# Kernel optimization log

Hardware: AMD Instinct MI355X
Metric: run time of the kernel (lower is better)

## Reference

```python
import jax, jax.numpy as jnp
import numpy as np

N_SRC = 50000
N_DST = 50000
N_EDGES = 600000
IN_FEAT = 128
OUT_FEAT = 128


def setup_inputs() -> dict:
    key = jax.random.key(0)
    k1, k2, k3, k4, k5, k6 = jax.random.split(key, 6)
    h_s = jax.random.normal(k1, (N_SRC, IN_FEAT), dtype=jnp.float32)
    h_d = jax.random.normal(k2, (N_DST, IN_FEAT), dtype=jnp.float32)
    src = jax.random.randint(k3, (N_EDGES,), 0, N_SRC, dtype=jnp.int32)
    dst = jax.random.randint(k4, (N_EDGES,), 0, N_DST, dtype=jnp.int32)
    # nn.Linear(in_feat*2, out_feat): W [out, 2*in], b [out]
    W = jax.random.normal(k5, (OUT_FEAT, 2 * IN_FEAT), dtype=jnp.float32) * 0.05
    b = jax.random.normal(k6, (OUT_FEAT,), dtype=jnp.float32) * 0.05
    return {"h_s": h_s, "h_d": h_d, "src": src, "dst": dst, "W": W, "b": b}


def reference(h_s, h_d, src, dst, W, b):
    # copy_u + mean: gather source features along edges, segment-mean by dst
    msgs = h_s[src]  # [E, in_feat]
    neigh_sum = jax.ops.segment_sum(msgs, dst, num_segments=N_DST)  # [n_dst, in_feat]
    deg = jax.ops.segment_sum(jnp.ones((src.shape[0],), dtype=h_s.dtype), dst,
                              num_segments=N_DST)
    h_neigh = neigh_sum / jnp.maximum(deg, 1.0)[:, None]  # zero-degree -> 0
    # concat + linear (dropout is identity in eval mode)
    feat = jnp.concatenate([h_d, h_neigh], axis=1)  # [n_dst, 2*in_feat]
    out = feat @ W.T + b  # [n_dst, out_feat]
    return out
```

## Files before the change

### kernel.cpp

```cpp
#include <hip/hip_runtime.h>
#include <hip/hip_bf16.h>

#define N_SRC 50000
#define N_DST 50000
#define N_EDGES 600000
#define IN_FEAT 128
#define OUT_FEAT 128
#define CAP 32
#define DEG_STRIDE 16

typedef __attribute__((ext_vector_type(8))) short short8;
typedef __attribute__((ext_vector_type(4))) float float4v;
typedef __attribute__((ext_vector_type(4))) float f32x4;
typedef __attribute__((ext_vector_type(4))) unsigned short ushort4v;

#define FILL_BLOCKS 2344
#define HS4 (N_SRC * IN_FEAT / 4)
#define CVT_BLOCKS (HS4 / 256)
#define W_BLOCKS 16
#define K1_GRID 15024

__global__ __launch_bounds__(256) void fill_cvt_kernel(
    const float* __restrict__ h_s, const float* __restrict__ h_d,
    const float* __restrict__ W,
    const int* __restrict__ src, const int* __restrict__ dst,
    int* __restrict__ deg, ushort* __restrict__ permu,
    ushort* __restrict__ hsb, ushort* __restrict__ hdb,
    ushort* __restrict__ wfrag)
{
    int bid = blockIdx.x;
    int tid = threadIdx.x;

    if (bid % 6 == 5) {
        int fb = bid / 6;
        if (fb >= FILL_BLOCKS) return;
        int e = fb * 256 + tid;
        if (e < N_EDGES) {
            int s = __builtin_nontemporal_load(src + e);
            int d = __builtin_nontemporal_load(dst + e);
            int p = atomicAdd(&deg[(size_t)d * DEG_STRIDE], 1);
            if (p < CAP) permu[(size_t)d * CAP + p] = (ushort)s;
        }
        return;
    }

    int cid = bid - bid / 6;

    if (cid < 2 * CVT_BLOCKS) {
        bool first = (cid < CVT_BLOCKS);
        const float* in = first ? h_s : h_d;
        ushort* outp    = first ? hsb : hdb;
        int idx = (first ? cid : cid - CVT_BLOCKS) * 256 + tid;
        f32x4 v = __builtin_nontemporal_load((const f32x4*)in + idx);
        __hip_bfloat16 o[4];
        o[0] = __float2bfloat16(v.x);
        o[1] = __float2bfloat16(v.y);
        o[2] = __float2bfloat16(v.z);
        o[3] = __float2bfloat16(v.w);
        __builtin_nontemporal_store(*(ushort4v*)o, (ushort4v*)(outp + (size_t)idx * 4));
        return;
    }
    int wb = cid - 2 * CVT_BLOCKS;
    if (wb >= W_BLOCKS) return;

    int c = wb * 256 + tid;
    int f  = c >> 6;
    int l  = c & 63;
    int ks = f >> 3;
    int nt = f & 7;
    int row = nt * 16 + (l & 15);
    int col = ks * 32 + (l >> 4) * 8;
    const float* wp = W + (size_t)row * 256 + col;
    f32x4 w0 = __builtin_nontemporal_load((const f32x4*)wp);
    f32x4 w1 = __builtin_nontemporal_load((const f32x4*)wp + 1);
    __hip_bfloat16 o[8];
    o[0] = __float2bfloat16(w0.x); o[1] = __float2bfloat16(w0.y);
    o[2] = __float2bfloat16(w0.z); o[3] = __float2bfloat16(w0.w);
    o[4] = __float2bfloat16(w1.x); o[5] = __float2bfloat16(w1.y);
    o[6] = __float2bfloat16(w1.z); o[7] = __float2bfloat16(w1.w);
    __builtin_nontemporal_store(*(short8*)o, (short8*)(wfrag + (size_t)c * 8));
}

__global__ __launch_bounds__(256) void gather_gemm_kernel(
    const ushort* __restrict__ hsb, const int* __restrict__ deg,
    const ushort* __restrict__ permu, const ushort* __restrict__ hdb,
    const ushort* __restrict__ wfrag, const float* __restrict__ b,
    float* __restrict__ out)
{
    __shared__ ushort sM[16 * 128];

    int tid  = threadIdx.x;
    int wave = tid >> 6;
    int lane = tid & 63;
    int lm   = lane & 15;
    int lq   = lane >> 4;
    int row0 = blockIdx.x * 16;

    for (int r = 0; r < 4; ++r) {
        int lr  = wave * 4 + r;
        int row = row0 + lr;
        int dg  = deg[(size_t)row * DEG_STRIDE];
        int dgr = (dg < CAP) ? dg : CAP;
        const ushort* prow = permu + (size_t)row * CAP;
        const ushort2* hp  = (const ushort2*)hsb;

        ushort4 p0 = *(const ushort4*)(prow);
        ushort4 p1 = *(const ushort4*)(prow + 4);
        ushort4 p2 = *(const ushort4*)(prow + 8);
        ushort4 p3 = *(const ushort4*)(prow + 12);
        int t[16] = {p0.x, p0.y, p0.z, p0.w, p1.x, p1.y, p1.z, p1.w,
                     p2.x, p2.y, p2.z, p2.w, p3.x, p3.y, p3.z, p3.w};

        float ax = 0.f, ay = 0.f;
        ushort2 u[16];
#pragma unroll
        for (int q = 0; q < 16; ++q) {
            int s = (q < dgr) ? t[q] : 0;
            u[q] = hp[(size_t)s * 64 + lane];
        }
#pragma unroll
        for (int q = 0; q < 16; ++q) {
            float m = (q < dgr) ? 1.f : 0.f;
            ax += m * __uint_as_float((unsigned)u[q].x << 16);
            ay += m * __uint_as_float((unsigned)u[q].y << 16);
        }
        for (int j = 16; j < dgr; j += 8) {
            ushort4 pa = *(const ushort4*)(prow + j);
            ushort4 pb = *(const ushort4*)(prow + j + 4);
            int tt[8] = {pa.x, pa.y, pa.z, pa.w, pb.x, pb.y, pb.z, pb.w};
            ushort2 v[8];
#pragma unroll
            for (int q = 0; q < 8; ++q) {
                int s = (j + q < dgr) ? tt[q] : 0;
                v[q] = hp[(size_t)s * 64 + lane];
            }
#pragma unroll
            for (int q = 0; q < 8; ++q) {
                float m = (j + q < dgr) ? 1.f : 0.f;
                ax += m * __uint_as_float((unsigned)v[q].x << 16);
                ay += m * __uint_as_float((unsigned)v[q].y << 16);
            }
        }

        float inv = (dg > 0) ? (1.0f / (float)dg) : 0.0f;
        __hip_bfloat16 ox = __float2bfloat16(ax * inv);
        __hip_bfloat16 oy = __float2bfloat16(ay * inv);
        unsigned pk = (unsigned)*(ushort*)&ox | ((unsigned)*(ushort*)&oy << 16);
        unsigned byte = ((unsigned)(lr * 256 + lane * 4)) ^ (((unsigned)lr & 7u) << 4);
        *(unsigned*)((char*)sM + byte) = pk;
    }
    __syncthreads();

    const ushort* ah = hdb + (size_t)(row0 + lm) * IN_FEAT + lq * 8;

    float4v acc[2];
    acc[0] = (float4v){0.f, 0.f, 0.f, 0.f};
    acc[1] = (float4v){0.f, 0.f, 0.f, 0.f};

#pragma unroll
    for (int ks = 0; ks < 8; ++ks) {
        short8 af;
        if (ks < 4) {
            af = __builtin_nontemporal_load((const short8*)(ah + ks * 32));
        } else {
            unsigned byte = ((unsigned)(lm * 256 + (((ks - 4) * 32 + lq * 8) * 2)))
                            ^ (((unsigned)lm & 7u) << 4);
            af = *(const short8*)((char*)sM + byte);
        }
#pragma unroll
        for (int j = 0; j < 2; ++j) {
            int nt = wave * 2 + j;
            short8 bf = *(const short8*)(wfrag + ((size_t)(ks * 8 + nt) * 64 + lane) * 8);
            acc[j] = __builtin_amdgcn_mfma_f32_16x16x32_bf16(af, bf, acc[j], 0, 0, 0);
        }
    }

#pragma unroll
    for (int j = 0; j < 2; ++j) {
        int nt  = wave * 2 + j;
        int col = nt * 16 + lm;
        float bias = b[col];
#pragma unroll
        for (int r = 0; r < 4; ++r) {
            int o = row0 + lq * 4 + r;
            __builtin_nontemporal_store(acc[j][r] + bias,
                                        out + (size_t)o * OUT_FEAT + col);
        }
    }
}

extern "C" void kernel_launch(void* const* d_in, const int* in_sizes, int n_in,
                              void* d_out, int out_size, void* d_ws, size_t ws_size,
                              hipStream_t stream) {
    const float* h_s = (const float*)d_in[0];
    const float* h_d = (const float*)d_in[1];
    const int*   src = (const int*)d_in[2];
    const int*   dst = (const int*)d_in[3];
    const float* W   = (const float*)d_in[4];
    const float* b   = (const float*)d_in[5];
    float* out = (float*)d_out;

    char* ws = (char*)d_ws;
    int*    deg    = (int*)ws;
    ushort* permu  = (ushort*)(ws + 3200000);
    ushort* hsb    = (ushort*)(ws + 6400000);
    ushort* hdb    = (ushort*)(ws + 19200000);
    ushort* wfrag  = (ushort*)(ws + 32000000);

    hipMemsetAsync(deg, 0, (size_t)N_DST * DEG_STRIDE * sizeof(int), stream);

    fill_cvt_kernel<<<K1_GRID, 256, 0, stream>>>(
        h_s, h_d, W, src, dst, deg, permu, hsb, hdb, wfrag);
    gather_gemm_kernel<<<N_DST / 16, 256, 0, stream>>>(
        hsb, deg, permu, hdb, wfrag, b, out);
}
```

Before: 171.6 us.

## Fuse fill/convert and gather-GEMM into one persistent kernel with grid barrier

Result: slower. 357.7 us (+108.5%).

```diff
diff --git a/kernel.cpp b/kernel.cpp
--- a/kernel.cpp
+++ b/kernel.cpp
@@ -9,183 +9,192 @@
 #define CAP 32
 #define DEG_STRIDE 16
 
+#define NBLK 1024
+#define NTHR 256
+#define NTHREADS (NBLK * NTHR)
+#define NTILES (N_DST / 16)
+#define HS4 (N_SRC * IN_FEAT / 4)
+
 typedef __attribute__((ext_vector_type(8))) short short8;
 typedef __attribute__((ext_vector_type(4))) float float4v;
 typedef __attribute__((ext_vector_type(4))) float f32x4;
 typedef __attribute__((ext_vector_type(4))) unsigned short ushort4v;
 
-#define FILL_BLOCKS 2344
-#define HS4 (N_SRC * IN_FEAT / 4)
-#define CVT_BLOCKS (HS4 / 256)
-#define W_BLOCKS 16
-#define K1_GRID 15024
-
-__global__ __launch_bounds__(256) void fill_cvt_kernel(
+__global__ __launch_bounds__(256, 4) void mega_kernel(
     const float* __restrict__ h_s, const float* __restrict__ h_d,
     const float* __restrict__ W,
     const int* __restrict__ src, const int* __restrict__ dst,
+    const float* __restrict__ b,
     int* __restrict__ deg, ushort* __restrict__ permu,
-    ushort* __restrict__ hsb, ushort* __restrict__ hdb,
-    ushort* __restrict__ wfrag)
+    ushort* __restrict__ hsb, ushort* __restrict__ wfrag,
+    int* __restrict__ bar, int* __restrict__ wcnt,
+    float* __restrict__ out)
 {
-    int bid = blockIdx.x;
+    __shared__ ushort sM[16 * 128];
+    __shared__ int sTile;
+
     int tid = threadIdx.x;
-
-    if (bid % 6 == 5) {
-        int fb = bid / 6;
-        if (fb >= FILL_BLOCKS) return;
-        int e = fb * 256 + tid;
-        if (e < N_EDGES) {
-            int s = __builtin_nontemporal_load(src + e);
-            int d = __builtin_nontemporal_load(dst + e);
-            int p = atomicAdd(&deg[(size_t)d * DEG_STRIDE], 1);
-            if (p < CAP) permu[(size_t)d * CAP + p] = (ushort)s;
-        }
-        return;
-    }
-
-    int cid = bid - bid / 6;
-
-    if (cid < 2 * CVT_BLOCKS) {
-        bool first = (cid < CVT_BLOCKS);
-        const float* in = first ? h_s : h_d;
-        ushort* outp    = first ? hsb : hdb;
-        int idx = (first ? cid : cid - CVT_BLOCKS) * 256 + tid;
-        f32x4 v = __builtin_nontemporal_load((const f32x4*)in + idx);
+    int gid = blockIdx.x * NTHR + tid;
+
+    for (int e = gid; e < N_EDGES; e += NTHREADS) {
+        int s = __builtin_nontemporal_load(src + e);
+        int d = __builtin_nontemporal_load(dst + e);
+        int p = atomicAdd(&deg[(size_t)d * DEG_STRIDE], 1);
+        if (p < CAP) permu[(size_t)d * CAP + p] = (ushort)s;
+    }
+
+    if (gid < 4096) {
+        int c  = gid;
+        int f  = c >> 6;
+        int l  = c & 63;
+        int ks = f >> 3;
+        int nt = f & 7;
+        int row = nt * 16 + (l & 15);
+        int col = ks * 32 + (l >> 4) * 8;
+        const float* wp = W + (size_t)row * 256 + col;
+        f32x4 w0 = __builtin_nontemporal_load((const f32x4*)wp);
+        f32x4 w1 = __builtin_nontemporal_load((const f32x4*)wp + 1);
+        __hip_bfloat16 o[8];
+        o[0] = __float2bfloat16(w0.x); o[1] = __float2bfloat16(w0.y);
+        o[2] = __float2bfloat16(w0.z); o[3] = __float2bfloat16(w0.w);
+        o[4] = __float2bfloat16(w1.x); o[5] = __float2bfloat16(w1.y);
+        o[6] = __float2bfloat16(w1.z); o[7] = __float2bfloat16(w1.w);
+        __builtin_nontemporal_store(*(short8*)o, (short8*)(wfrag + (size_t)c * 8));
+    }
+
+    for (int idx = gid; idx < HS4; idx += NTHREADS) {
+        f32x4 v = __builtin_nontemporal_load((const f32x4*)h_s + idx);
         __hip_bfloat16 o[4];
         o[0] = __float2bfloat16(v.x);
         o[1] = __float2bfloat16(v.y);
         o[2] = __float2bfloat16(v.z);
         o[3] = __float2bfloat16(v.w);
-        __builtin_nontemporal_store(*(ushort4v*)o, (ushort4v*)(outp + (size_t)idx * 4));
-        return;
-    }
-    int wb = cid - 2 * CVT_BLOCKS;
-    if (wb >= W_BLOCKS) return;
-
-    int c = wb * 256 + tid;
-    int f  = c >> 6;
-    int l  = c & 63;
-    int ks = f >> 3;
-    int nt = f & 7;
-    int row = nt * 16 + (l & 15);
-    int col = ks * 32 + (l >> 4) * 8;
-    const float* wp = W + (size_t)row * 256 + col;
-    f32x4 w0 = __builtin_nontemporal_load((const f32x4*)wp);
-    f32x4 w1 = __builtin_nontemporal_load((const f32x4*)wp + 1);
-    __hip_bfloat16 o[8];
-    o[0] = __float2bfloat16(w0.x); o[1] = __float2bfloat16(w0.y);
-    o[2] = __float2bfloat16(w0.z); o[3] = __float2bfloat16(w0.w);
-    o[4] = __float2bfloat16(w1.x); o[5] = __float2bfloat16(w1.y);
-    o[6] = __float2bfloat16(w1.z); o[7] = __float2bfloat16(w1.w);
-    __builtin_nontemporal_store(*(short8*)o, (short8*)(wfrag + (size_t)c * 8));
-}
-
-__global__ __launch_bounds__(256) void gather_gemm_kernel(
-    const ushort* __restrict__ hsb, const int* __restrict__ deg,
-    const ushort* __restrict__ permu, const ushort* __restrict__ hdb,
-    const ushort* __restrict__ wfrag, const float* __restrict__ b,
-    float* __restrict__ out)
-{
-    __shared__ ushort sM[16 * 128];
-
-    int tid  = threadIdx.x;
+        __builtin_nontemporal_store(*(ushort4v*)o, (ushort4v*)(hsb + (size_t)idx * 4));
+    }
+
+    __syncthreads();
+    if (tid == 0) {
+        __threadfence();
+        atomicAdd(bar, 1);
+        while (__hip_atomic_load(bar, __ATOMIC_RELAXED,
+                                 __HIP_MEMORY_SCOPE_AGENT) < NBLK)
+            __builtin_amdgcn_s_sleep(32);
+    }
+    __syncthreads();
+    __threadfence();
+
     int wave = tid >> 6;
     int lane = tid & 63;
     int lm   = lane & 15;
     int lq   = lane >> 4;
-    int row0 = blockIdx.x * 16;
-
-    for (int r = 0; r < 4; ++r) {
-        int lr  = wave * 4 + r;
-        int row = row0 + lr;
-        int dg  = deg[(size_t)row * DEG_STRIDE];
-        int dgr = (dg < CAP) ? dg : CAP;
-        const ushort* prow = permu + (size_t)row * CAP;
-        const ushort2* hp  = (const ushort2*)hsb;
-
-        ushort4 p0 = *(const ushort4*)(prow);
-        ushort4 p1 = *(const ushort4*)(prow + 4);
-        ushort4 p2 = *(const ushort4*)(prow + 8);
-        ushort4 p3 = *(const ushort4*)(prow + 12);
-        int t[16] = {p0.x, p0.y, p0.z, p0.w, p1.x, p1.y, p1.z, p1.w,
-                     p2.x, p2.y, p2.z, p2.w, p3.x, p3.y, p3.z, p3.w};
-
-        float ax = 0.f, ay = 0.f;
-        ushort2 u[16];
-#pragma unroll
-        for (int q = 0; q < 16; ++q) {
-            int s = (q < dgr) ? t[q] : 0;
-            u[q] = hp[(size_t)s * 64 + lane];
+
+    while (true) {
+        __syncthreads();
+        if (tid == 0) sTile = atomicAdd(wcnt, 1);
+        __syncthreads();
+        int t = sTile;
+        if (t >= NTILES) break;
+        int row0 = t * 16;
+
+        for (int r = 0; r < 4; ++r) {
+            int lr  = wave * 4 + r;
+            int row = row0 + lr;
+            int dg  = deg[(size_t)row * DEG_STRIDE];
+            int dgr = (dg < CAP) ? dg : CAP;
+            const ushort* prow = permu + (size_t)row * CAP;
+            const ushort2* hp  = (const ushort2*)hsb;
+
+            ushort4 p0 = *(const ushort4*)(prow);
+            ushort4 p1 = *(const ushort4*)(prow + 4);
+            ushort4 p2 = *(const ushort4*)(prow + 8);
+            ushort4 p3 = *(const ushort4*)(prow + 12);
+            int tt[16] = {p0.x, p0.y, p0.z, p0.w, p1.x, p1.y, p1.z, p1.w,
+                          p2.x, p2.y, p2.z, p2.w, p3.x, p3.y, p3.z, p3.w};
+
+            float ax = 0.f, ay = 0.f;
+            ushort2 u[16];
+#pragma unroll
+            for (int q = 0; q < 16; ++q) {
+                int s = (q < dgr) ? tt[q] : 0;
+                u[q] = hp[(size_t)s * 64 + lane];
+            }
+#pragma unroll
+            for (int q = 0; q < 16; ++q) {
+                float m = (q < dgr) ? 1.f : 0.f;
+                ax += m * __uint_as_float((unsigned)u[q].x << 16);
+                ay += m * __uint_as_float((unsigned)u[q].y << 16);
+            }
+            for (int j = 16; j < dgr; j += 8) {
+                ushort4 pa = *(const ushort4*)(prow + j);
+                ushort4 pb = *(const ushort4*)(prow + j + 4);
+                int t8[8] = {pa.x, pa.y, pa.z, pa.w, pb.x, pb.y, pb.z, pb.w};
+                ushort2 v[8];
+#pragma unroll
+                for (int q = 0; q < 8; ++q) {
+                    int s = (j + q < dgr) ? t8[q] : 0;
+                    v[q] = hp[(size_t)s * 64 + lane];
+                }
+#pragma unroll
+                for (int q = 0; q < 8; ++q) {
+                    float m = (j + q < dgr) ? 1.f : 0.f;
+                    ax += m * __uint_as_float((unsigned)v[q].x << 16);
+                    ay += m * __uint_as_float((unsigned)v[q].y << 16);
+                }
+            }
+
+            float inv = (dg > 0) ? (1.0f / (float)dg) : 0.0f;
+            __hip_bfloat16 ox = __float2bfloat16(ax * inv);
+            __hip_bfloat16 oy = __float2bfloat16(ay * inv);
+            unsigned pk = (unsigned)*(ushort*)&ox | ((unsigned)*(ushort*)&oy << 16);
+            unsigned byte = ((unsigned)(lr * 256 + lane * 4)) ^ (((unsigned)lr & 7u) << 4);
+            *(unsigned*)((char*)sM + byte) = pk;
         }
-#pragma unroll
-        for (int q = 0; q < 16; ++q) {
-            float m = (q < dgr) ? 1.f : 0.f;
-            ax += m * __uint_as_float((unsigned)u[q].x << 16);
-            ay += m * __uint_as_float((unsigned)u[q].y << 16);
+        __syncthreads();
+
+        const float* ad = h_d + (size_t)(row0 + lm) * IN_FEAT + lq * 8;
+
+        float4v acc[2];
+        acc[0] = (float4v){0.f, 0.f, 0.f, 0.f};
+        acc[1] = (float4v){0.f, 0.f, 0.f, 0.f};
+
+#pragma unroll
+        for (int ks = 0; ks < 8; ++ks) {
+            short8 af;
+            if (ks < 4) {
+                f32x4 q0 = __builtin_nontemporal_load((const f32x4*)(ad + ks * 32));
+                f32x4 q1 = __builtin_nontemporal_load((const f32x4*)(ad + ks * 32) + 1);
+                __hip_bfloat16 o[8];
+                o[0] = __float2bfloat16(q0.x); o[1] = __float2bfloat16(q0.y);
+                o[2] = __float2bfloat16(q0.z); o[3] = __float2bfloat16(q0.w);
+                o[4] = __float2bfloat16(q1.x); o[5] = __float2bfloat16(q1.y);
+                o[6] = __float2bfloat16(q1.z); o[7] = __float2bfloat16(q1.w);
+                af = *(short8*)o;
+            } else {
+                unsigned byte = ((unsigned)(lm * 256 + (((ks - 4) * 32 + lq * 8) * 2)))
+                                ^ (((unsigned)lm & 7u) << 4);
+                af = *(const short8*)((char*)sM + byte);
+            }
+#pragma unroll
+            for (int j = 0; j < 2; ++j) {
+                int nt = wave * 2 + j;
+                short8 bf = *(const short8*)(wfrag + ((size_t)(ks * 8 + nt) * 64 + lane) * 8);
+                acc[j] = __builtin_amdgcn_mfma_f32_16x16x32_bf16(af, bf, acc[j], 0, 0, 0);
+            }
         }
-        for (int j = 16; j < dgr; j += 8) {
-            ushort4 pa = *(const ushort4*)(prow + j);
-            ushort4 pb = *(const ushort4*)(prow + j + 4);
-            int tt[8] = {pa.x, pa.y, pa.z, pa.w, pb.x, pb.y, pb.z, pb.w};
-            ushort2 v[8];
-#pragma unroll
-            for (int q = 0; q < 8; ++q) {
-                int s = (j + q < dgr) ? tt[q] : 0;
-                v[q] = hp[(size_t)s * 64 + lane];
-            }
-#pragma unroll
-            for (int q = 0; q < 8; ++q) {
-                float m = (j + q < dgr) ? 1.f : 0.f;
-                ax += m * __uint_as_float((unsigned)v[q].x << 16);
-                ay += m * __uint_as_float((unsigned)v[q].y << 16);
+
+#pragma unroll
+        for (int j = 0; j < 2; ++j) {
+            int nt  = wave * 2 + j;
+            int col = nt * 16 + lm;
+            float bias = b[col];
+#pragma unroll
+            for (int r = 0; r < 4; ++r) {
+                int o = row0 + lq * 4 + r;
+                __builtin_nontemporal_store(acc[j][r] + bias,
+                                            out + (size_t)o * OUT_FEAT + col);
             }
         }
-
-        float inv = (dg > 0) ? (1.0f / (float)dg) : 0.0f;
-        __hip_bfloat16 ox = __float2bfloat16(ax * inv);
-        __hip_bfloat16 oy = __float2bfloat16(ay * inv);
-        unsigned pk = (unsigned)*(ushort*)&ox | ((unsigned)*(ushort*)&oy << 16);
-        unsigned byte = ((unsigned)(lr * 256 + lane * 4)) ^ (((unsigned)lr & 7u) << 4);
-        *(unsigned*)((char*)sM + byte) = pk;
-    }
-    __syncthreads();
-
-    const ushort* ah = hdb + (size_t)(row0 + lm) * IN_FEAT + lq * 8;
-
-    float4v acc[2];
-    acc[0] = (float4v){0.f, 0.f, 0.f, 0.f};
-    acc[1] = (float4v){0.f, 0.f, 0.f, 0.f};
-
-#pragma unroll
-    for (int ks = 0; ks < 8; ++ks) {
-        short8 af;
-        if (ks < 4) {
-            af = __builtin_nontemporal_load((const short8*)(ah + ks * 32));
-        } else {
-            unsigned byte = ((unsigned)(lm * 256 + (((ks - 4) * 32 + lq * 8) * 2)))
-                            ^ (((unsigned)lm & 7u) << 4);
-            af = *(const short8*)((char*)sM + byte);
-        }
-#pragma unroll
-        for (int j = 0; j < 2; ++j) {
-            int nt = wave * 2 + j;
-            short8 bf = *(const short8*)(wfrag + ((size_t)(ks * 8 + nt) * 64 + lane) * 8);
-            acc[j] = __builtin_amdgcn_mfma_f32_16x16x32_bf16(af, bf, acc[j], 0, 0, 0);
-        }
-    }
-
-#pragma unroll
-    for (int j = 0; j < 2; ++j) {
-        int nt  = wave * 2 + j;
-        int col = nt * 16 + lm;
-        float bias = b[col];
-#pragma unroll
-        for (int r = 0; r < 4; ++r) {
-            int o = row0 + lq * 4 + r;
-            __builtin_nontemporal_store(acc[j][r] + bias,
-                                        out + (size_t)o * OUT_FEAT + col);
-        }
+        __syncthreads();
     }
 }
 
@@ -202,15 +211,14 @@
 
     char* ws = (char*)d_ws;
     int*    deg    = (int*)ws;
-    ushort* permu  = (ushort*)(ws + 3200000);
-    ushort* hsb    = (ushort*)(ws + 6400000);
-    ushort* hdb    = (ushort*)(ws + 19200000);
-    ushort* wfrag  = (ushort*)(ws + 32000000);
-
-    hipMemsetAsync(deg, 0, (size_t)N_DST * DEG_STRIDE * sizeof(int), stream);
-
-    fill_cvt_kernel<<<K1_GRID, 256, 0, stream>>>(
-        h_s, h_d, W, src, dst, deg, permu, hsb, hdb, wfrag);
-    gather_gemm_kernel<<<N_DST / 16, 256, 0, stream>>>(
-        hsb, deg, permu, hdb, wfrag, b, out);
+    int*    bar    = (int*)(ws + 3200000);
+    int*    wcnt   = (int*)(ws + 3200004);
+    ushort* permu  = (ushort*)(ws + 3200128);
+    ushort* hsb    = (ushort*)(ws + 6400128);
+    ushort* wfrag  = (ushort*)(ws + 19200128);
+
+    hipMemsetAsync(ws, 0, 3200008, stream);
+
+    mega_kernel<<<NBLK, NTHR, 0, stream>>>(
+        h_s, h_d, W, src, dst, b, deg, permu, hsb, wfrag, bar, wcnt, out);
 }
```

## Partition degree counters and neighbor buckets per XCD to localize atomics

Applied to the files above, without the earlier changes.

Result: slower. 190.4 us (+11.0%).

```diff
diff --git a/kernel.cpp b/kernel.cpp
--- a/kernel.cpp
+++ b/kernel.cpp
@@ -6,8 +6,8 @@
 #define N_EDGES 600000
 #define IN_FEAT 128
 #define OUT_FEAT 128
-#define CAP 32
-#define DEG_STRIDE 16
+#define CAPX 16
+#define NXCD 8
 
 typedef __attribute__((ext_vector_type(8))) short short8;
 typedef __attribute__((ext_vector_type(4))) float float4v;
@@ -19,6 +19,8 @@
 #define CVT_BLOCKS (HS4 / 256)
 #define W_BLOCKS 16
 #define K1_GRID 15024
+
+#define XCC_GETREG_IMM (20 | (3 << 11))
 
 __global__ __launch_bounds__(256) void fill_cvt_kernel(
     const float* __restrict__ h_s, const float* __restrict__ h_d,
@@ -34,12 +36,14 @@
     if (bid % 6 == 5) {
         int fb = bid / 6;
         if (fb >= FILL_BLOCKS) return;
+        unsigned x = __builtin_amdgcn_s_getreg(XCC_GETREG_IMM) & 7u;
         int e = fb * 256 + tid;
         if (e < N_EDGES) {
             int s = __builtin_nontemporal_load(src + e);
             int d = __builtin_nontemporal_load(dst + e);
-            int p = atomicAdd(&deg[(size_t)d * DEG_STRIDE], 1);
-            if (p < CAP) permu[(size_t)d * CAP + p] = (ushort)s;
+            size_t cell = (size_t)x * N_DST + d;
+            int p = atomicAdd(&deg[cell], 1);
+            if (p < CAPX) permu[cell * CAPX + p] = (ushort)s;
         }
         return;
     }
@@ -96,49 +100,64 @@
     int lq   = lane >> 4;
     int row0 = blockIdx.x * 16;
 
+    const ushort2* hp = (const ushort2*)hsb;
+
     for (int r = 0; r < 4; ++r) {
         int lr  = wave * 4 + r;
         int row = row0 + lr;
-        int dg  = deg[(size_t)row * DEG_STRIDE];
-        int dgr = (dg < CAP) ? dg : CAP;
-        const ushort* prow = permu + (size_t)row * CAP;
-        const ushort2* hp  = (const ushort2*)hsb;
-
-        ushort4 p0 = *(const ushort4*)(prow);
-        ushort4 p1 = *(const ushort4*)(prow + 4);
-        ushort4 p2 = *(const ushort4*)(prow + 8);
-        ushort4 p3 = *(const ushort4*)(prow + 12);
-        int t[16] = {p0.x, p0.y, p0.z, p0.w, p1.x, p1.y, p1.z, p1.w,
-                     p2.x, p2.y, p2.z, p2.w, p3.x, p3.y, p3.z, p3.w};
+
+        int     cc[8];
+        ushort4 pa[8];
+#pragma unroll
+        for (int x = 0; x < 8; ++x) {
+            size_t cell = (size_t)x * N_DST + row;
+            cc[x] = deg[cell];
+            pa[x] = *(const ushort4*)(permu + cell * CAPX);
+        }
+        int dg = 0;
+#pragma unroll
+        for (int x = 0; x < 8; ++x) dg += cc[x];
 
         float ax = 0.f, ay = 0.f;
-        ushort2 u[16];
-#pragma unroll
-        for (int q = 0; q < 16; ++q) {
-            int s = (q < dgr) ? t[q] : 0;
-            u[q] = hp[(size_t)s * 64 + lane];
-        }
-#pragma unroll
-        for (int q = 0; q < 16; ++q) {
-            float m = (q < dgr) ? 1.f : 0.f;
-            ax += m * __uint_as_float((unsigned)u[q].x << 16);
-            ay += m * __uint_as_float((unsigned)u[q].y << 16);
-        }
-        for (int j = 16; j < dgr; j += 8) {
-            ushort4 pa = *(const ushort4*)(prow + j);
-            ushort4 pb = *(const ushort4*)(prow + j + 4);
-            int tt[8] = {pa.x, pa.y, pa.z, pa.w, pb.x, pb.y, pb.z, pb.w};
-            ushort2 v[8];
-#pragma unroll
-            for (int q = 0; q < 8; ++q) {
-                int s = (j + q < dgr) ? tt[q] : 0;
-                v[q] = hp[(size_t)s * 64 + lane];
+#pragma unroll
+        for (int x = 0; x < 8; ++x) {
+            int cx = __builtin_amdgcn_readfirstlane(cc[x] < CAPX ? cc[x] : CAPX);
+            if (cx <= 0) continue;
+            int t4[4] = {pa[x].x, pa[x].y, pa[x].z, pa[x].w};
+            ushort2 u[4];
+#pragma unroll
+            for (int q = 0; q < 4; ++q) {
+                int s = (q < cx) ? t4[q] : 0;
+                u[q] = hp[(size_t)s * 64 + lane];
             }
 #pragma unroll
-            for (int q = 0; q < 8; ++q) {
-                float m = (j + q < dgr) ? 1.f : 0.f;
-                ax += m * __uint_as_float((unsigned)v[q].x << 16);
-                ay += m * __uint_as_float((unsigned)v[q].y << 16);
+            for (int q = 0; q < 4; ++q) {
+                float m = (q < cx) ? 1.f : 0.f;
+                ax += m * __uint_as_float((unsigned)u[q].x << 16);
+                ay += m * __uint_as_float((unsigned)u[q].y << 16);
+            }
+            if (cx > 4) {
+                const ushort* prow = permu + ((size_t)x * N_DST + row) * CAPX;
+                ushort4 pb = *(const ushort4*)(prow + 4);
+                int t2[4] = {pb.x, pb.y, pb.z, pb.w};
+                ushort2 v[4];
+#pragma unroll
+                for (int q = 0; q < 4; ++q) {
+                    int s = (4 + q < cx) ? t2[q] : 0;
+                    v[q] = hp[(size_t)s * 64 + lane];
+                }
+#pragma unroll
+                for (int q = 0; q < 4; ++q) {
+                    float m = (4 + q < cx) ? 1.f : 0.f;
+                    ax += m * __uint_as_float((unsigned)v[q].x << 16);
+                    ay += m * __uint_as_float((unsigned)v[q].y << 16);
+                }
+                for (int q = 8; q < cx; ++q) {
+                    int s = prow[q];
+                    ushort2 w = hp[(size_t)s * 64 + lane];
+                    ax += __uint_as_float((unsigned)w.x << 16);
+                    ay += __uint_as_float((unsigned)w.y << 16);
+                }
             }
         }
 
@@ -202,12 +221,12 @@
 
     char* ws = (char*)d_ws;
     int*    deg    = (int*)ws;
-    ushort* permu  = (ushort*)(ws + 3200000);
-    ushort* hsb    = (ushort*)(ws + 6400000);
-    ushort* hdb    = (ushort*)(ws + 19200000);
-    ushort* wfrag  = (ushort*)(ws + 32000000);
-
-    hipMemsetAsync(deg, 0, (size_t)N_DST * DEG_STRIDE * sizeof(int), stream);
+    ushort* permu  = (ushort*)(ws + 1600000);
+    ushort* hsb    = (ushort*)(ws + 14400000);
+    ushort* hdb    = (ushort*)(ws + 27200000);
+    ushort* wfrag  = (ushort*)(ws + 40000000);
+
+    hipMemsetAsync(deg, 0, (size_t)NXCD * N_DST * sizeof(int), stream);
 
     fill_cvt_kernel<<<K1_GRID, 256, 0, stream>>>(
         h_s, h_d, W, src, dst, deg, permu, hsb, hdb, wfrag);
```
